# Kernel optimization log

Hardware: AMD Instinct MI355X
Metric: run time of the kernel (lower is better)

## Reference

```python
import jax, jax.numpy as jnp
import numpy as np

B, S, H, SSZ, IN = 1024, 100, 128, 100, 2


def _gru(x, h, Wih, Whh, bih, bhh):
    # PyTorch GRU cell: gates ordered (reset, update, new)
    gx = x @ Wih.T + bih
    gh = h @ Whh.T + bhh
    xr, xz, xn = jnp.split(gx, 3, axis=-1)
    hr, hz, hn = jnp.split(gh, 3, axis=-1)
    r = jax.nn.sigmoid(xr + hr)
    z = jax.nn.sigmoid(xz + hz)
    n = jnp.tanh(xn + r * hn)
    return (1.0 - z) * n + z * h


def _attn(inst_h, rnn_out, W, v):
    # inst_h: [B,S,H], rnn_out: [B,H] -> softmax attention weights [B,S]
    h = jnp.concatenate([inst_h, jnp.broadcast_to(rnn_out[:, None, :], inst_h.shape)], axis=-1)
    s = jax.nn.relu(jnp.einsum('bsk,kh->bsh', h, W)) @ v
    return jax.nn.softmax(s, axis=1)


def setup_inputs() -> dict:
    key = jax.random.key(0)
    k = jax.random.split(key, 32)
    p = lambda i, shape, sc=0.05: sc * jax.random.normal(k[i], shape, jnp.float32)
    instance = jax.random.uniform(k[0], (B, S, IN), jnp.float32)
    # solutions must be per-row permutations of node indices
    solution_1 = jnp.argsort(jax.random.uniform(k[1], (B, S)), axis=1).astype(jnp.int32)
    solution_2 = jnp.argsort(jax.random.uniform(k[2], (B, S)), axis=1).astype(jnp.int32)
    eps = jax.random.normal(k[3], (B, SSZ), jnp.float32)
    return dict(
        instance=instance, solution_1=solution_1, solution_2=solution_2, eps=eps,
        emb_i_W=p(4, (H, IN)), emb_i_b=jnp.zeros(H, jnp.float32),
        emb_r_W=p(5, (H, IN)), emb_r_b=jnp.zeros(H, jnp.float32),
        attn_W=p(6, (2 * H, H)), attn_v=p(7, (H,)),
        gru_Wih=p(8, (3 * H, H)), gru_Whh=p(9, (3 * H, H)),
        gru_bih=jnp.zeros(3 * H, jnp.float32), gru_bhh=jnp.zeros(3 * H, jnp.float32),
        grud_Wih=p(10, (3 * H, 2 * H)), grud_Whh=p(11, (3 * H, H)),
        grud_bih=jnp.zeros(3 * H, jnp.float32), grud_bhh=jnp.zeros(3 * H, jnp.float32),
        enc_fc1_W=p(12, (SSZ, H)), enc_fc1_b=jnp.zeros(SSZ, jnp.float32),
        enc_fc2_W=p(13, (SSZ, H)), enc_fc2_b=jnp.zeros(SSZ, jnp.float32),
        ptr_W=p(14, (2 * H, H)), ptr_v=p(15, (H,)),
        pfc1_W=p(16, (2 * H, 2 * H + SSZ)), pfc1_b=jnp.zeros(2 * H, jnp.float32),
        pfc2_W=p(17, (H, 2 * H)), pfc2_b=jnp.zeros(H, jnp.float32),
    )


def reference(instance, solution_1, solution_2, eps,
              emb_i_W, emb_i_b, emb_r_W, emb_r_b, attn_W, attn_v,
              gru_Wih, gru_Whh, gru_bih, gru_bhh,
              grud_Wih, grud_Whh, grud_bih, grud_bhh,
              enc_fc1_W, enc_fc1_b, enc_fc2_W, enc_fc2_b,
              ptr_W, ptr_v, pfc1_W, pfc1_b, pfc2_W, pfc2_b):
    b_idx = jnp.arange(B)
    inst_h = instance @ emb_i_W.T + emb_i_b  # [B,S,H]
    emb_r = lambda x: x @ emb_r_W.T + emb_r_b
    take = lambda ptr: instance[b_idx, ptr]  # gather node coords [B,IN]

    # ---------------- Encoder ----------------
    def enc_step(carry, ptr):
        h1, h2, ref_h = carry
        h1 = _gru(ref_h, h1, gru_Wih, gru_Whh, gru_bih, gru_bhh)
        a = _attn(inst_h, h1, attn_W, attn_v)
        context = jnp.einsum('bs,bsh->bh', a, inst_h)
        ref_h = emb_r(take(ptr))
        rnn_in = jnp.concatenate([ref_h, context], axis=-1)  # [B,2H]
        h2 = _gru(rnn_in, h2, grud_Wih, grud_Whh, grud_bih, grud_bhh)
        return (h1, h2, ref_h), None

    z0 = jnp.zeros((B, H), instance.dtype)
    ref_h0 = emb_r(take(solution_1[:, 0]))
    (_, h2, _), _ = jax.lax.scan(enc_step, (z0, z0, ref_h0), solution_1[:, 1:].T)
    mu = h2 @ enc_fc1_W.T + enc_fc1_b
    log_var = h2 @ enc_fc2_W.T + enc_fc2_b
    Z = mu + eps * jnp.exp(0.5 * log_var)

    # ---------------- Decoder (teacher forcing) ----------------
    mask0 = jnp.ones((B, S), instance.dtype).at[b_idx, solution_2[:, 0]].set(0.0)

    def dec_step(carry, ptr):
        h1, ref_in, mask = carry
        ref_h = emb_r(ref_in)
        h1 = _gru(ref_h, h1, gru_Wih, gru_Whh, gru_bih, gru_bhh)
        a = _attn(inst_h, h1, attn_W, attn_v)
        context = jnp.einsum('bs,bsh->bh', a, inst_h)
        fc_in = jnp.concatenate([context, Z, ref_h], axis=-1)  # [B, 2H+SSZ]
        fc_out = (fc_in @ pfc1_W.T + pfc1_b) @ pfc2_W.T + pfc2_b  # no activation, as in torch
        hcat = jnp.concatenate([inst_h, jnp.broadcast_to(fc_out[:, None, :], inst_h.shape)], axis=-1)
        logits = jnp.tanh(jnp.einsum('bsk,kh->bsh', hcat, ptr_W)) @ ptr_v  # [B,S]
        probs = jax.nn.softmax(logits + jnp.log(mask), axis=1)
        logp = jnp.log(probs[b_idx, ptr])
        pred = jnp.argmax(probs, axis=1)
        mask = mask.at[b_idx, ptr].set(0.0)  # tsp.update_mask: mark chosen node visited
        return (h1, take(ptr), mask), (pred, logp)

    init = (z0, take(solution_2[:, 0]), mask0)
    _, (preds, logps) = jax.lax.scan(dec_step, init, solution_2[:, 1:].T)
    tour_idx = jnp.concatenate([solution_2[:, :1], preds.T.astype(solution_2.dtype)], axis=1)
    tour_logp = logps.T  # [B, S-1]
    return (mu, log_var, Z, tour_idx, tour_logp)
```

## Files before the change

### kernel.cpp

```cpp
#include <hip/hip_runtime.h>
#include <math.h>

static constexpr int NB  = 1024;
static constexpr int NS  = 100;
static constexpr int NH  = 128;
static constexpr int GPB = 2;
static constexpr int NTHR = 256;
static constexpr int NBLK = NB / GPB;
static constexpr int CH  = 4;

static constexpr int OUT_MU = 0;
static constexpr int OUT_LV = NB * NS;
static constexpr int OUT_Z  = 2 * NB * NS;
static constexpr int OUT_TI = 3 * NB * NS;
static constexpr int OUT_LP = 4 * NB * NS;

#define NEGF (-3.4e38f)

template<int C4>
__device__ __forceinline__ void dot2x3f(const float* __restrict__ wr0,
        const float* __restrict__ wr1, const float* __restrict__ wr2,
        const float* __restrict__ x0, const float* __restrict__ x1,
        float& r00, float& r01, float& r10, float& r11, float& r20, float& r21)
{
    const float4* W0 = reinterpret_cast<const float4*>(wr0);
    const float4* W1 = reinterpret_cast<const float4*>(wr1);
    const float4* W2 = reinterpret_cast<const float4*>(wr2);
    const float4* X0 = reinterpret_cast<const float4*>(x0);
    const float4* X1 = reinterpret_cast<const float4*>(x1);
    float a00 = 0.f, a01 = 0.f, a10 = 0.f, a11 = 0.f, a20 = 0.f, a21 = 0.f;
    #pragma unroll 4
    for (int c = 0; c < C4; ++c) {
        float4 u0 = W0[c], u1 = W1[c], u2 = W2[c];
        float4 v0 = X0[c], v1 = X1[c];
        a00 = fmaf(u0.x, v0.x, a00); a00 = fmaf(u0.y, v0.y, a00); a00 = fmaf(u0.z, v0.z, a00); a00 = fmaf(u0.w, v0.w, a00);
        a01 = fmaf(u0.x, v1.x, a01); a01 = fmaf(u0.y, v1.y, a01); a01 = fmaf(u0.z, v1.z, a01); a01 = fmaf(u0.w, v1.w, a01);
        a10 = fmaf(u1.x, v0.x, a10); a10 = fmaf(u1.y, v0.y, a10); a10 = fmaf(u1.z, v0.z, a10); a10 = fmaf(u1.w, v0.w, a10);
        a11 = fmaf(u1.x, v1.x, a11); a11 = fmaf(u1.y, v1.y, a11); a11 = fmaf(u1.z, v1.z, a11); a11 = fmaf(u1.w, v1.w, a11);
        a20 = fmaf(u2.x, v0.x, a20); a20 = fmaf(u2.y, v0.y, a20); a20 = fmaf(u2.z, v0.z, a20); a20 = fmaf(u2.w, v0.w, a20);
        a21 = fmaf(u2.x, v1.x, a21); a21 = fmaf(u2.y, v1.y, a21); a21 = fmaf(u2.z, v1.z, a21); a21 = fmaf(u2.w, v1.w, a21);
    }
    r00 = a00; r01 = a01; r10 = a10; r11 = a11; r20 = a20; r21 = a21;
}

template<int C4>
__device__ __forceinline__ void dot2f(const float* __restrict__ w,
        const float* __restrict__ x0, const float* __restrict__ x1, float& r0, float& r1)
{
    const float4* W = reinterpret_cast<const float4*>(w);
    const float4* X0 = reinterpret_cast<const float4*>(x0);
    const float4* X1 = reinterpret_cast<const float4*>(x1);
    float a0 = 0.f, a1 = 0.f;
    #pragma unroll 8
    for (int c = 0; c < C4; ++c) {
        float4 u = W[c];
        float4 v0 = X0[c], v1 = X1[c];
        a0 = fmaf(u.x, v0.x, a0); a0 = fmaf(u.y, v0.y, a0); a0 = fmaf(u.z, v0.z, a0); a0 = fmaf(u.w, v0.w, a0);
        a1 = fmaf(u.x, v1.x, a1); a1 = fmaf(u.y, v1.y, a1); a1 = fmaf(u.z, v1.z, a1); a1 = fmaf(u.w, v1.w, a1);
    }
    r0 = a0; r1 = a1;
}

template<int C4>
__device__ __forceinline__ double dotwd(const float* __restrict__ w, const float* __restrict__ x)
{
    const float4* W = reinterpret_cast<const float4*>(w);
    double a = 0.0;
    #pragma unroll 8
    for (int c = 0; c < C4; ++c) {
        float4 u = W[c];
        const float* p = x + 4 * c;
        a = fma((double)u.x, (double)p[0], a);
        a = fma((double)u.y, (double)p[1], a);
        a = fma((double)u.z, (double)p[2], a);
        a = fma((double)u.w, (double)p[3], a);
    }
    return a;
}

__device__ __forceinline__ void gruc(const float* __restrict__ bih, const float* __restrict__ bhh,
        const float* __restrict__ pa, const float* __restrict__ pb, float* __restrict__ h, int j)
{
    double r = 1.0 / (1.0 + exp(-(((double)pa[j]        + (double)bih[j])        + ((double)pb[j]        + (double)bhh[j]))));
    double z = 1.0 / (1.0 + exp(-(((double)pa[NH + j]   + (double)bih[NH + j])   + ((double)pb[NH + j]   + (double)bhh[NH + j]))));
    double n = tanh(((double)pa[2*NH + j] + (double)bih[2*NH + j]) + r * ((double)pb[2*NH + j] + (double)bhh[2*NH + j]));
    h[j] = (float)((1.0 - z) * n + z * (double)h[j]);
}

__device__ __forceinline__ void qhalf(const float* __restrict__ col, int k0,
        const float* __restrict__ hA, const float* __restrict__ hB, double& r0, double& r1)
{
    double a00=0.0,a01=0.0,a02=0.0,a03=0.0;
    double a10=0.0,a11=0.0,a12=0.0,a13=0.0;
    #pragma unroll 8
    for (int k = 0; k < 64; k += 4) {
        float w0 = col[(size_t)(k0+k+0) * NH];
        float w1 = col[(size_t)(k0+k+1) * NH];
        float w2 = col[(size_t)(k0+k+2) * NH];
        float w3 = col[(size_t)(k0+k+3) * NH];
        float4 h0 = *reinterpret_cast<const float4*>(&hA[k0+k]);
        float4 h1v = *reinterpret_cast<const float4*>(&hB[k0+k]);
        a00 = fma((double)w0, (double)h0.x, a00);
        a01 = fma((double)w1, (double)h0.y, a01);
        a02 = fma((double)w2, (double)h0.z, a02);
        a03 = fma((double)w3, (double)h0.w, a03);
        a10 = fma((double)w0, (double)h1v.x, a10);
        a11 = fma((double)w1, (double)h1v.y, a11);
        a12 = fma((double)w2, (double)h1v.z, a12);
        a13 = fma((double)w3, (double)h1v.w, a13);
    }
    r0 = (a00+a01)+(a02+a03); r1 = (a10+a11)+(a12+a13);
}

__device__ __forceinline__ float relu_head(const double* __restrict__ qh,
        const double2* __restrict__ dA, const float* __restrict__ va, float c0v, float c1v)
{
    double c00 = (double)c0v, c10 = (double)c1v;
    double acc0=0.0,acc1=0.0,acc2=0.0,acc3=0.0;
    #pragma unroll 4
    for (int h = 0; h < NH; h += 4) {
        double2 A0=dA[h+0],A1=dA[h+1],A2=dA[h+2],A3=dA[h+3];
        double p0 = fma(c00,A0.x,fma(c10,A0.y,qh[h+0]));
        double p1 = fma(c00,A1.x,fma(c10,A1.y,qh[h+1]));
        double p2 = fma(c00,A2.x,fma(c10,A2.y,qh[h+2]));
        double p3 = fma(c00,A3.x,fma(c10,A3.y,qh[h+3]));
        acc0 = fma(fmax(p0,0.0),(double)va[h+0],acc0);
        acc1 = fma(fmax(p1,0.0),(double)va[h+1],acc1);
        acc2 = fma(fmax(p2,0.0),(double)va[h+2],acc2);
        acc3 = fma(fmax(p3,0.0),(double)va[h+3],acc3);
    }
    return (float)((acc0+acc1)+(acc2+acc3));
}

__device__ __forceinline__ float tanh_head(const double* __restrict__ qh,
        const double2* __restrict__ dA, const float* __restrict__ vp, float c0v, float c1v)
{
    double c00 = (double)c0v, c10 = (double)c1v;
    double acc0=0.0,acc1=0.0,acc2=0.0,acc3=0.0;
    #pragma unroll 4
    for (int h = 0; h < NH; h += 4) {
        double2 A0=dA[h+0],A1=dA[h+1],A2=dA[h+2],A3=dA[h+3];
        double p0 = fma(c00,A0.x,fma(c10,A0.y,qh[h+0]));
        double p1 = fma(c00,A1.x,fma(c10,A1.y,qh[h+1]));
        double p2 = fma(c00,A2.x,fma(c10,A2.y,qh[h+2]));
        double p3 = fma(c00,A3.x,fma(c10,A3.y,qh[h+3]));
        acc0 = fma((double)tanhf((float)p0),(double)vp[h+0],acc0);
        acc1 = fma((double)tanhf((float)p1),(double)vp[h+1],acc1);
        acc2 = fma((double)tanhf((float)p2),(double)vp[h+2],acc2);
        acc3 = fma((double)tanhf((float)p3),(double)vp[h+3],acc3);
    }
    return (float)((acc0+acc1)+(acc2+acc3));
}

__device__ __forceinline__ float ctx_chain(const float* __restrict__ a,
        const float* __restrict__ c0, const float* __restrict__ c1,
        float w0, float w1, float bb)
{
    double a0=0.0,a1=0.0,a2=0.0,a3=0.0;
    #pragma unroll 5
    for (int s = 0; s < NS; s += 4) {
        float ih0 = fmaf(c0[s+0], w0, fmaf(c1[s+0], w1, bb));
        float ih1 = fmaf(c0[s+1], w0, fmaf(c1[s+1], w1, bb));
        float ih2 = fmaf(c0[s+2], w0, fmaf(c1[s+2], w1, bb));
        float ih3 = fmaf(c0[s+3], w0, fmaf(c1[s+3], w1, bb));
        a0 += (double)a[s+0] * (double)ih0;
        a1 += (double)a[s+1] * (double)ih1;
        a2 += (double)a[s+2] * (double)ih2;
        a3 += (double)a[s+3] * (double)ih3;
    }
    return (float)((a0+a1)+(a2+a3));
}

__global__ __launch_bounds__(NTHR) void vae_v21(
    const float* __restrict__ instance, const int* __restrict__ sol1,
    const int* __restrict__ sol2, const float* __restrict__ eps,
    const float* __restrict__ emb_i_W, const float* __restrict__ emb_i_b,
    const float* __restrict__ emb_r_W, const float* __restrict__ emb_r_b,
    const float* __restrict__ attn_W, const float* __restrict__ attn_v,
    const float* __restrict__ gru_Wih, const float* __restrict__ gru_Whh,
    const float* __restrict__ gru_bih, const float* __restrict__ gru_bhh,
    const float* __restrict__ grud_Wih, const float* __restrict__ grud_Whh,
    const float* __restrict__ grud_bih, const float* __restrict__ grud_bhh,
    const float* __restrict__ efc1_W, const float* __restrict__ efc1_b,
    const float* __restrict__ efc2_W, const float* __restrict__ efc2_b,
    const float* __restrict__ ptr_W, const float* __restrict__ ptr_v,
    const float* __restrict__ pfc1_W, const float* __restrict__ pfc1_b,
    const float* __restrict__ pfc2_W, const float* __restrict__ pfc2_b,
    float* __restrict__ out)
{
    __shared__ __align__(16) float  s_x[GPB][360];
    __shared__ __align__(16) float  s_h1[GPB][NH], s_h2[GPB][NH];
    __shared__ float  s_pa[GPB][3 * NH], s_pb[GPB][3 * NH];
    __shared__ double2 dAa[NH], dAp[NH];
    __shared__ double dAba[NH], dAbp[NH];
    __shared__ float  s_c0[GPB][NS], s_c1[GPB][NS];
    __shared__ float  t_wi0[NH], t_wi1[NH], t_bi[NH];
    __shared__ float  t_wr0[NH], t_wr1[NH], t_br[NH];
    __shared__ float  t_va[NH], t_vp[NH];
    __shared__ float  t_gbih[3*NH], t_gbhh[3*NH], t_dbih[3*NH], t_dbhh[3*NH];
    __shared__ float  t_p1b[256], t_p2b[NH];
    __shared__ int    s_sol1[GPB][NS], s_sol2[GPB][NS];
    __shared__ __align__(16) float  s_ref[GPB][NH];
    __shared__ __align__(16) float  h1buf[CH][GPB][NH];
    __shared__ float    rcb0[GPB][CH+1], rcb1[GPB][CH+1];
    __shared__ unsigned maskb[CH][GPB][4], m_run[GPB][4];
    __shared__ __align__(16) double d_qh[CH][GPB][NH];
    __shared__ __align__(16) float  d_pl[2*CH][NS];
    __shared__ __align__(16) float  d_x[2*CH][360];
    __shared__ __align__(16) float  d_fch[2*CH][256];
    __shared__ __align__(16) float  d_fco[CH][GPB][NH];

    const int tid = threadIdx.x;
    const int bbase = blockIdx.x * GPB;
    const int j = tid & (NH - 1);
    const int half = tid >> 7;
    const int g = half;
    const int lane = tid & 63;

    if (tid < NH) {
        t_wi0[tid] = emb_i_W[2*tid]; t_wi1[tid] = emb_i_W[2*tid+1]; t_bi[tid] = emb_i_b[tid];
        t_wr0[tid] = emb_r_W[2*tid]; t_wr1[tid] = emb_r_W[2*tid+1]; t_br[tid] = emb_r_b[tid];
        t_va[tid] = attn_v[tid]; t_vp[tid] = ptr_v[tid];
        t_p2b[tid] = pfc2_b[tid];
    }
    t_p1b[tid] = pfc1_b[tid];
    for (int i = tid; i < 3 * NH; i += NTHR) {
        t_gbih[i] = gru_bih[i]; t_gbhh[i] = gru_bhh[i];
        t_dbih[i] = grud_bih[i]; t_dbhh[i] = grud_bhh[i];
    }
    for (int i = tid; i < GPB * NS; i += NTHR) {
        int gg = i / NS, s = i - gg * NS;
        s_c0[gg][s] = instance[(size_t)((bbase + gg) * NS + s) * 2 + 0];
        s_c1[gg][s] = instance[(size_t)((bbase + gg) * NS + s) * 2 + 1];
        s_sol1[gg][s] = sol1[(bbase + gg) * NS + s];
        s_sol2[gg][s] = sol2[(bbase + gg) * NS + s];
    }
    s_h1[g][j] = 0.f;
    s_h2[g][j] = 0.f;
    __syncthreads();
    {
        const float* Wm = (half == 0) ? attn_W : ptr_W;
        double a0 = 0.0, a1 = 0.0, ab = 0.0;
        for (int k = 0; k < NH; ++k) {
            double wv2 = (double)Wm[(size_t)k * NH + j];
            a0 = fma((double)t_wi0[k], wv2, a0);
            a1 = fma((double)t_wi1[k], wv2, a1);
            ab = fma((double)t_bi[k],  wv2, ab);
        }
        if (half == 0) { dAa[j].x = a0; dAa[j].y = a1; dAba[j] = ab; }
        else           { dAp[j].x = a0; dAp[j].y = a1; dAbp[j] = ab; }
    }
    {
        int sp = s_sol1[g][0];
        s_ref[g][j] = fmaf(s_c0[g][sp], t_wr0[j], fmaf(s_c1[g][sp], t_wr1[j], t_br[j]));
    }
    __syncthreads();

    for (int c = 0; c < (NS - 1 + CH - 1) / CH; ++c) {
        const int t0 = 1 + c * CH;
        const int CHc = (t0 + CH <= NS) ? CH : (NS - t0);
        if (tid < GPB) {
            const int gg = tid;
            for (int qi = 0; qi < CHc; ++qi) {
                int sp = s_sol1[gg][t0 + qi];
                rcb0[gg][qi] = s_c0[gg][sp];
                rcb1[gg][qi] = s_c1[gg][sp];
            }
        }
        __syncthreads();
        for (int q = 0; q < CHc; ++q) {
            if (half == 0) {
                float a00,a01,a10,a11,a20,a21;
                dot2x3f<32>(gru_Wih + (size_t)j * NH, gru_Wih + (size_t)(NH + j) * NH,
                            gru_Wih + (size_t)(2*NH + j) * NH, s_ref[0], s_ref[1],
                            a00,a01,a10,a11,a20,a21);
                s_pa[0][j] = a00;        s_pa[1][j] = a01;
                s_pa[0][NH + j] = a10;   s_pa[1][NH + j] = a11;
                s_pa[0][2*NH + j] = a20; s_pa[1][2*NH + j] = a21;
            } else {
                float a00,a01,a10,a11,a20,a21;
                dot2x3f<32>(gru_Whh + (size_t)j * NH, gru_Whh + (size_t)(NH + j) * NH,
                            gru_Whh + (size_t)(2*NH + j) * NH, s_h1[0], s_h1[1],
                            a00,a01,a10,a11,a20,a21);
                s_pb[0][j] = a00;        s_pb[1][j] = a01;
                s_pb[0][NH + j] = a10;   s_pb[1][NH + j] = a11;
                s_pb[0][2*NH + j] = a20; s_pb[1][2*NH + j] = a21;
            }
            __syncthreads();
            gruc(t_gbih, t_gbhh, s_pa[g], s_pb[g], s_h1[g], j);
            h1buf[q][g][j] = s_h1[g][j];
            s_ref[g][j] = fmaf(rcb0[g][q], t_wr0[j], fmaf(rcb1[g][q], t_wr1[j], t_br[j]));
            __syncthreads();
        }
        {
            const float* col = attn_W + (size_t)NH * NH + j;
            for (int tt = (tid >> 7); tt < CHc; tt += 2) {
                double qA0, qA1, qB0, qB1;
                qhalf(col, 0,  h1buf[tt][0], h1buf[tt][1], qA0, qA1);
                qhalf(col, 64, h1buf[tt][0], h1buf[tt][1], qB0, qB1);
                d_qh[tt][0][j] = dAba[j] + (qA0 + qB0);
                d_qh[tt][1][j] = dAba[j] + (qA1 + qB1);
            }
        }
        __syncthreads();
        for (int idx = tid; idx < 2 * CHc * NS; idx += NTHR) {
            int task = idx / NS, s = idx - task * NS;
            int tt = task >> 1, gg = task & 1;
            d_pl[task][s] = relu_head(d_qh[tt][gg], dAa, t_va, s_c0[gg][s], s_c1[gg][s]);
        }
        __syncthreads();
        {
            int w = tid >> 6;
            for (int task = w; task < 2 * CHc; task += 4) {
                float v1 = d_pl[task][lane];
                bool hasHi = (lane + 64 < NS);
                float v2 = hasHi ? d_pl[task][lane + 64] : NEGF;
                float m = fmaxf(v1, v2);
                m = fmaxf(m, __shfl_xor(m, 32)); m = fmaxf(m, __shfl_xor(m, 16));
                m = fmaxf(m, __shfl_xor(m, 8));  m = fmaxf(m, __shfl_xor(m, 4));
                m = fmaxf(m, __shfl_xor(m, 2));  m = fmaxf(m, __shfl_xor(m, 1));
                float f1 = (float)exp((double)v1 - (double)m);
                float f2 = 0.f;
                if (hasHi) f2 = (float)exp((double)v2 - (double)m);
                double ps = (double)f1 + (double)f2;
                ps += __shfl_xor(ps, 32); ps += __shfl_xor(ps, 16);
                ps += __shfl_xor(ps, 8);  ps += __shfl_xor(ps, 4);
                ps += __shfl_xor(ps, 2);  ps += __shfl_xor(ps, 1);
                d_pl[task][lane] = (float)((double)f1 / ps);
                if (hasHi) d_pl[task][lane + 64] = (float)((double)f2 / ps);
            }
        }
        __syncthreads();
        for (int idx = tid; idx < 2 * CHc * NH; idx += NTHR) {
            int task = idx >> 7, jj = idx & 127;
            int tt = task >> 1, gg = task & 1;
            d_x[task][NH + jj] = ctx_chain(d_pl[task], s_c0[gg], s_c1[gg], t_wi0[jj], t_wi1[jj], t_bi[jj]);
            d_x[task][jj] = fmaf(rcb0[gg][tt], t_wr0[jj], fmaf(rcb1[gg][tt], t_wr1[jj], t_br[jj]));
        }
        __syncthreads();
        for (int q = 0; q < CHc; ++q) {
            if (half == 0) {
                float a00,a01,a10,a11,a20,a21;
                dot2x3f<64>(grud_Wih + (size_t)j * 256, grud_Wih + (size_t)(NH + j) * 256,
                            grud_Wih + (size_t)(2*NH + j) * 256, d_x[2*q], d_x[2*q+1],
                            a00,a01,a10,a11,a20,a21);
                s_pa[0][j] = a00;        s_pa[1][j] = a01;
                s_pa[0][NH + j] = a10;   s_pa[1][NH + j] = a11;
                s_pa[0][2*NH + j] = a20; s_pa[1][2*NH + j] = a21;
            } else {
                float a00,a01,a10,a11,a20,a21;
                dot2x3f<32>(grud_Whh + (size_t)j * NH, grud_Whh + (size_t)(NH + j) * NH,
                            grud_Whh + (size_t)(2*NH + j) * NH, s_h2[0], s_h2[1],
                            a00,a01,a10,a11,a20,a21);
                s_pb[0][j] = a00;        s_pb[1][j] = a01;
                s_pb[0][NH + j] = a10;   s_pb[1][NH + j] = a11;
                s_pb[0][2*NH + j] = a20; s_pb[1][2*NH + j] = a21;
            }
            __syncthreads();
            gruc(t_dbih, t_dbhh, s_pa[g], s_pb[g], s_h2[g], j);
            __syncthreads();
        }
    }

    for (int idx = tid; idx < GPB * NS; idx += NTHR) {
        int gg = idx / NS, s = idx - gg * NS, b = bbase + gg;
        double mu = dotwd<32>(efc1_W + (size_t)s * NH, s_h2[gg]) + (double)efc1_b[s];
        double lv = dotwd<32>(efc2_W + (size_t)s * NH, s_h2[gg]) + (double)efc2_b[s];
        double z  = mu + (double)eps[(size_t)b * NS + s] * exp(0.5 * lv);
        out[OUT_MU + b * NS + s] = (float)mu;
        out[OUT_LV + b * NS + s] = (float)lv;
        out[OUT_Z  + b * NS + s] = (float)z;
        s_x[gg][NH + s] = (float)z;
    }
    s_h1[g][j] = 0.f;
    __syncthreads();
    if (tid < GPB) {
        int b = bbase + tid;
        int s0 = s_sol2[tid][0];
        m_run[tid][0] = 0xFFFFFFFFu; m_run[tid][1] = 0xFFFFFFFFu;
        m_run[tid][2] = 0xFFFFFFFFu; m_run[tid][3] = 0xFu;
        m_run[tid][s0 >> 5] &= ~(1u << (s0 & 31));
        out[OUT_TI + b * NS + 0] = (float)s0;
    }
    __syncthreads();
    {
        int p0 = s_sol2[g][0];
        s_ref[g][j] = fmaf(s_c0[g][p0], t_wr0[j], fmaf(s_c1[g][p0], t_wr1[j], t_br[j]));
    }
    __syncthreads();

    for (int c = 0; c < (NS - 1 + CH - 1) / CH; ++c) {
        const int t0 = 1 + c * CH;
        const int CHc = (t0 + CH <= NS) ? CH : (NS - t0);
        if (tid < GPB) {
            const int gg = tid;
            for (int qi = 0; qi <= CHc; ++qi) {
                int tt = t0 + qi;
                if (qi < CHc) {
                    maskb[qi][gg][0] = m_run[gg][0];
                    maskb[qi][gg][1] = m_run[gg][1];
                    maskb[qi][gg][2] = m_run[gg][2];
                    maskb[qi][gg][3] = m_run[gg][3];
                    int pt = s_sol2[gg][tt];
                    m_run[gg][pt >> 5] &= ~(1u << (pt & 31));
                }
                int sp = s_sol2[gg][tt - 1];
                rcb0[gg][qi] = s_c0[gg][sp];
                rcb1[gg][qi] = s_c1[gg][sp];
            }
        }
        __syncthreads();
        for (int q = 0; q < CHc; ++q) {
            if (half == 0) {
                float a00,a01,a10,a11,a20,a21;
                dot2x3f<32>(gru_Wih + (size_t)j * NH, gru_Wih + (size_t)(NH + j) * NH,
                            gru_Wih + (size_t)(2*NH + j) * NH, s_ref[0], s_ref[1],
                            a00,a01,a10,a11,a20,a21);
                s_pa[0][j] = a00;        s_pa[1][j] = a01;
                s_pa[0][NH + j] = a10;   s_pa[1][NH + j] = a11;
                s_pa[0][2*NH + j] = a20; s_pa[1][2*NH + j] = a21;
            } else {
                float a00,a01,a10,a11,a20,a21;
                dot2x3f<32>(gru_Whh + (size_t)j * NH, gru_Whh + (size_t)(NH + j) * NH,
                            gru_Whh + (size_t)(2*NH + j) * NH, s_h1[0], s_h1[1],
                            a00,a01,a10,a11,a20,a21);
                s_pb[0][j] = a00;        s_pb[1][j] = a01;
                s_pb[0][NH + j] = a10;   s_pb[1][NH + j] = a11;
                s_pb[0][2*NH + j] = a20; s_pb[1][2*NH + j] = a21;
            }
            __syncthreads();
            gruc(t_gbih, t_gbhh, s_pa[g], s_pb[g], s_h1[g], j);
            h1buf[q][g][j] = s_h1[g][j];
            s_ref[g][j] = fmaf(rcb0[g][q+1], t_wr0[j], fmaf(rcb1[g][q+1], t_wr1[j], t_br[j]));
            __syncthreads();
        }
        {
            const float* col = attn_W + (size_t)NH * NH + j;
            for (int tt = (tid >> 7); tt < CHc; tt += 2) {
                double qA0, qA1, qB0, qB1;
                qhalf(col, 0,  h1buf[tt][0], h1buf[tt][1], qA0, qA1);
                qhalf(col, 64, h1buf[tt][0], h1buf[tt][1], qB0, qB1);
                d_qh[tt][0][j] = dAba[j] + (qA0 + qB0);
                d_qh[tt][1][j] = dAba[j] + (qA1 + qB1);
            }
        }
        __syncthreads();
        for (int idx = tid; idx < 2 * CHc * NS; idx += NTHR) {
            int task = idx / NS, s = idx - task * NS;
            int tt = task >> 1, gg = task & 1;
            d_pl[task][s] = relu_head(d_qh[tt][gg], dAa, t_va, s_c0[gg][s], s_c1[gg][s]);
        }
        __syncthreads();
        {
            int w = tid >> 6;
            for (int task = w; task < 2 * CHc; task += 4) {
                float v1 = d_pl[task][lane];
                bool hasHi = (lane + 64 < NS);
                float v2 = hasHi ? d_pl[task][lane + 64] : NEGF;
                float m = fmaxf(v1, v2);
                m = fmaxf(m, __shfl_xor(m, 32)); m = fmaxf(m, __shfl_xor(m, 16));
                m = fmaxf(m, __shfl_xor(m, 8));  m = fmaxf(m, __shfl_xor(m, 4));
                m = fmaxf(m, __shfl_xor(m, 2));  m = fmaxf(m, __shfl_xor(m, 1));
                float f1 = (float)exp((double)v1 - (double)m);
                float f2 = 0.f;
                if (hasHi) f2 = (float)exp((double)v2 - (double)m);
                double ps = (double)f1 + (double)f2;
                ps += __shfl_xor(ps, 32); ps += __shfl_xor(ps, 16);
                ps += __shfl_xor(ps, 8);  ps += __shfl_xor(ps, 4);
                ps += __shfl_xor(ps, 2);  ps += __shfl_xor(ps, 1);
                d_pl[task][lane] = (float)((double)f1 / ps);
                if (hasHi) d_pl[task][lane + 64] = (float)((double)f2 / ps);
            }
        }
        __syncthreads();
        for (int idx = tid; idx < 2 * CHc * NH; idx += NTHR) {
            int task = idx >> 7, jj = idx & 127;
            int tt = task >> 1, gg = task & 1;
            d_x[task][jj] = ctx_chain(d_pl[task], s_c0[gg], s_c1[gg], t_wi0[jj], t_wi1[jj], t_bi[jj]);
            float rc0 = rcb0[gg][tt], rc1 = rcb1[gg][tt];
            d_x[task][228 + jj] = fmaf(rc0, t_wr0[jj], fmaf(rc1, t_wr1[jj], t_br[jj]));
        }
        for (int idx = tid; idx < 2 * CHc * NS; idx += NTHR) {
            int task = idx / NS, s = idx - task * NS;
            int gg = task & 1;
            d_x[task][NH + s] = s_x[gg][NH + s];
        }
        __syncthreads();
        {
            const float* wrow = pfc1_W + (size_t)tid * 356;
            float bb = t_p1b[tid];
            for (int tt = 0; tt < CHc; ++tt) {
                float r0, r1;
                dot2f<89>(wrow, d_x[2*tt], d_x[2*tt+1], r0, r1);
                d_fch[2*tt][tid] = r0 + bb; d_fch[2*tt+1][tid] = r1 + bb;
            }
        }
        __syncthreads();
        {
            const float* wrow = pfc2_W + (size_t)j * 256;
            for (int tt = (tid >> 7); tt < CHc; tt += 2) {
                float r0, r1;
                dot2f<64>(wrow, d_fch[2*tt], d_fch[2*tt+1], r0, r1);
                d_fco[tt][0][j] = r0 + t_p2b[j];
                d_fco[tt][1][j] = r1 + t_p2b[j];
            }
        }
        __syncthreads();
        {
            const float* col = ptr_W + (size_t)NH * NH + j;
            for (int tt = (tid >> 7); tt < CHc; tt += 2) {
                double qA0, qA1, qB0, qB1;
                qhalf(col, 0,  d_fco[tt][0], d_fco[tt][1], qA0, qA1);
                qhalf(col, 64, d_fco[tt][0], d_fco[tt][1], qB0, qB1);
                d_qh[tt][0][j] = dAbp[j] + (qA0 + qB0);
                d_qh[tt][1][j] = dAbp[j] + (qA1 + qB1);
            }
        }
        __syncthreads();
        for (int idx = tid; idx < 2 * CHc * NS; idx += NTHR) {
            int task = idx / NS, s = idx - task * NS;
            int tt = task >> 1, gg = task & 1;
            d_pl[task][s] = tanh_head(d_qh[tt][gg], dAp, t_vp, s_c0[gg][s], s_c1[gg][s]);
        }
        __syncthreads();
        {
            int w = tid >> 6;
            for (int task = w; task < 2 * CHc; task += 4) {
                int tt = task >> 1, gg = task & 1, tstep = t0 + tt;
                const unsigned* mwp = &maskb[tt][gg][0];
                bool u1 = (mwp[lane >> 5] >> (lane & 31)) & 1u;
                float l1 = d_pl[task][lane];
                float c1v = u1 ? l1 : NEGF;
                bool u2 = false; float l2 = 0.f, c2v = NEGF;
                if (lane + 64 < NS) {
                    u2 = (mwp[(lane + 64) >> 5] >> (lane & 31)) & 1u;
                    l2 = d_pl[task][lane + 64];
                    c2v = u2 ? l2 : NEGF;
                }
                float m = fmaxf(c1v, c2v);
                m = fmaxf(m, __shfl_xor(m, 32)); m = fmaxf(m, __shfl_xor(m, 16));
                m = fmaxf(m, __shfl_xor(m, 8));  m = fmaxf(m, __shfl_xor(m, 4));
                m = fmaxf(m, __shfl_xor(m, 2));  m = fmaxf(m, __shfl_xor(m, 1));
                float f1 = u1 ? (float)exp((double)l1 - (double)m) : 0.f;
                float f2 = (lane + 64 < NS && u2) ? (float)exp((double)l2 - (double)m) : 0.f;
                float bv = f1; int bi = lane;
                if (lane + 64 < NS && f2 > bv) { bv = f2; bi = lane + 64; }
                double ps = (double)f1 + (double)f2;
                #pragma unroll
                for (int o = 32; o >= 1; o >>= 1) {
                    float  ov = __shfl_xor(bv, o);
                    int    oi = __shfl_xor(bi, o);
                    double op = __shfl_xor(ps, o);
                    ps += op;
                    if (ov > bv || (ov == bv && oi < bi)) { bv = ov; bi = oi; }
                }
                int pt = s_sol2[gg][tstep];
                float a1s = __shfl(f1, pt & 63);
                float a2s = __shfl(f2, pt & 63);
                float a_pt = (pt < 64) ? a1s : a2s;
                if (lane == 0) {
                    int b2 = bbase + gg;
                    double logp = log((double)a_pt / ps);
                    out[OUT_TI + (size_t)b2 * NS + tstep]             = (float)bi;
                    out[OUT_LP + (size_t)b2 * (NS - 1) + (tstep - 1)] = (float)logp;
                }
            }
        }
        __syncthreads();
    }
}

extern "C" void kernel_launch(void* const* d_in, const int* in_sizes, int n_in,
                              void* d_out, int out_size, void* d_ws, size_t ws_size,
                              hipStream_t stream)
{
    (void)in_sizes; (void)n_in; (void)out_size; (void)d_ws; (void)ws_size;
    vae_v21<<<NBLK, NTHR, 0, stream>>>(
        (const float*)d_in[0], (const int*)d_in[1], (const int*)d_in[2], (const float*)d_in[3],
        (const float*)d_in[4], (const float*)d_in[5], (const float*)d_in[6], (const float*)d_in[7],
        (const float*)d_in[8], (const float*)d_in[9], (const float*)d_in[10], (const float*)d_in[11],
        (const float*)d_in[12], (const float*)d_in[13], (const float*)d_in[14], (const float*)d_in[15],
        (const float*)d_in[16], (const float*)d_in[17], (const float*)d_in[18], (const float*)d_in[19],
        (const float*)d_in[20], (const float*)d_in[21], (const float*)d_in[22], (const float*)d_in[23],
        (const float*)d_in[24], (const float*)d_in[25], (const float*)d_in[26], (const float*)d_in[27],
        (float*)d_out);
}
```

Baseline: 11.58 ms.

## Compute full GRU cell per thread to drop one barrier per step

Each thread now computes all three input-side and hidden-side gate dot products for its own (group, hidden unit) and applies the GRU update in registers. This removes the shared s_pa/s_pb staging and one __syncthreads per recurrent step. Reference embeddings for a whole chunk are precomputed in parallel before the loop, and hidden states are ping-ponged through h1buf. The cost is that each weight row is now read by both groups separately, giving more weight traffic per thread and no reuse of a weight load across the two batch rows.

```diff
diff --git a/kernel.cpp b/kernel.cpp
--- a/kernel.cpp
+++ b/kernel.cpp
@@ -18,29 +18,24 @@
 #define NEGF (-3.4e38f)
 
 template<int C4>
-__device__ __forceinline__ void dot2x3f(const float* __restrict__ wr0,
+__device__ __forceinline__ void dot1x3f(const float* __restrict__ wr0,
         const float* __restrict__ wr1, const float* __restrict__ wr2,
-        const float* __restrict__ x0, const float* __restrict__ x1,
-        float& r00, float& r01, float& r10, float& r11, float& r20, float& r21)
+        const float* __restrict__ x, float& r0, float& r1, float& r2)
 {
     const float4* W0 = reinterpret_cast<const float4*>(wr0);
     const float4* W1 = reinterpret_cast<const float4*>(wr1);
     const float4* W2 = reinterpret_cast<const float4*>(wr2);
-    const float4* X0 = reinterpret_cast<const float4*>(x0);
-    const float4* X1 = reinterpret_cast<const float4*>(x1);
-    float a00 = 0.f, a01 = 0.f, a10 = 0.f, a11 = 0.f, a20 = 0.f, a21 = 0.f;
+    const float4* X  = reinterpret_cast<const float4*>(x);
+    float a0 = 0.f, a1 = 0.f, a2 = 0.f;
     #pragma unroll 4
     for (int c = 0; c < C4; ++c) {
         float4 u0 = W0[c], u1 = W1[c], u2 = W2[c];
-        float4 v0 = X0[c], v1 = X1[c];
-        a00 = fmaf(u0.x, v0.x, a00); a00 = fmaf(u0.y, v0.y, a00); a00 = fmaf(u0.z, v0.z, a00); a00 = fmaf(u0.w, v0.w, a00);
-        a01 = fmaf(u0.x, v1.x, a01); a01 = fmaf(u0.y, v1.y, a01); a01 = fmaf(u0.z, v1.z, a01); a01 = fmaf(u0.w, v1.w, a01);
-        a10 = fmaf(u1.x, v0.x, a10); a10 = fmaf(u1.y, v0.y, a10); a10 = fmaf(u1.z, v0.z, a10); a10 = fmaf(u1.w, v0.w, a10);
-        a11 = fmaf(u1.x, v1.x, a11); a11 = fmaf(u1.y, v1.y, a11); a11 = fmaf(u1.z, v1.z, a11); a11 = fmaf(u1.w, v1.w, a11);
-        a20 = fmaf(u2.x, v0.x, a20); a20 = fmaf(u2.y, v0.y, a20); a20 = fmaf(u2.z, v0.z, a20); a20 = fmaf(u2.w, v0.w, a20);
-        a21 = fmaf(u2.x, v1.x, a21); a21 = fmaf(u2.y, v1.y, a21); a21 = fmaf(u2.z, v1.z, a21); a21 = fmaf(u2.w, v1.w, a21);
-    }
-    r00 = a00; r01 = a01; r10 = a10; r11 = a11; r20 = a20; r21 = a21;
+        float4 v = X[c];
+        a0 = fmaf(u0.x, v.x, a0); a0 = fmaf(u0.y, v.y, a0); a0 = fmaf(u0.z, v.z, a0); a0 = fmaf(u0.w, v.w, a0);
+        a1 = fmaf(u1.x, v.x, a1); a1 = fmaf(u1.y, v.y, a1); a1 = fmaf(u1.z, v.z, a1); a1 = fmaf(u1.w, v.w, a1);
+        a2 = fmaf(u2.x, v.x, a2); a2 = fmaf(u2.y, v.y, a2); a2 = fmaf(u2.z, v.z, a2); a2 = fmaf(u2.w, v.w, a2);
+    }
+    r0 = a0; r1 = a1; r2 = a2;
 }
 
 template<int C4>
@@ -78,13 +73,13 @@
     return a;
 }
 
-__device__ __forceinline__ void gruc(const float* __restrict__ bih, const float* __restrict__ bhh,
-        const float* __restrict__ pa, const float* __restrict__ pb, float* __restrict__ h, int j)
-{
-    double r = 1.0 / (1.0 + exp(-(((double)pa[j]        + (double)bih[j])        + ((double)pb[j]        + (double)bhh[j]))));
-    double z = 1.0 / (1.0 + exp(-(((double)pa[NH + j]   + (double)bih[NH + j])   + ((double)pb[NH + j]   + (double)bhh[NH + j]))));
-    double n = tanh(((double)pa[2*NH + j] + (double)bih[2*NH + j]) + r * ((double)pb[2*NH + j] + (double)bhh[2*NH + j]));
-    h[j] = (float)((1.0 - z) * n + z * (double)h[j]);
+__device__ __forceinline__ float grucr(const float* __restrict__ bih, const float* __restrict__ bhh,
+        float pa0, float pa1, float pa2, float pb0, float pb1, float pb2, float hold, int j)
+{
+    double r = 1.0 / (1.0 + exp(-(((double)pa0 + (double)bih[j])      + ((double)pb0 + (double)bhh[j]))));
+    double z = 1.0 / (1.0 + exp(-(((double)pa1 + (double)bih[NH + j]) + ((double)pb1 + (double)bhh[NH + j]))));
+    double n = tanh(((double)pa2 + (double)bih[2*NH + j]) + r * ((double)pb2 + (double)bhh[2*NH + j]));
+    return (float)((1.0 - z) * n + z * (double)hold);
 }
 
 __device__ __forceinline__ void qhalf(const float* __restrict__ col, int k0,
@@ -171,7 +166,7 @@
     return (float)((a0+a1)+(a2+a3));
 }
 
-__global__ __launch_bounds__(NTHR) void vae_v21(
+__global__ __launch_bounds__(NTHR) void vae_v22(
     const float* __restrict__ instance, const int* __restrict__ sol1,
     const int* __restrict__ sol2, const float* __restrict__ eps,
     const float* __restrict__ emb_i_W, const float* __restrict__ emb_i_b,
@@ -190,7 +185,6 @@
 {
     __shared__ __align__(16) float  s_x[GPB][360];
     __shared__ __align__(16) float  s_h1[GPB][NH], s_h2[GPB][NH];
-    __shared__ float  s_pa[GPB][3 * NH], s_pb[GPB][3 * NH];
     __shared__ double2 dAa[NH], dAp[NH];
     __shared__ double dAba[NH], dAbp[NH];
     __shared__ float  s_c0[GPB][NS], s_c1[GPB][NS];
@@ -200,7 +194,7 @@
     __shared__ float  t_gbih[3*NH], t_gbhh[3*NH], t_dbih[3*NH], t_dbhh[3*NH];
     __shared__ float  t_p1b[256], t_p2b[NH];
     __shared__ int    s_sol1[GPB][NS], s_sol2[GPB][NS];
-    __shared__ __align__(16) float  s_ref[GPB][NH];
+    __shared__ __align__(16) float  refs[CH][GPB][NH];
     __shared__ __align__(16) float  h1buf[CH][GPB][NH];
     __shared__ float    rcb0[GPB][CH+1], rcb1[GPB][CH+1];
     __shared__ unsigned maskb[CH][GPB][4], m_run[GPB][4];
@@ -250,10 +244,6 @@
         if (half == 0) { dAa[j].x = a0; dAa[j].y = a1; dAba[j] = ab; }
         else           { dAp[j].x = a0; dAp[j].y = a1; dAbp[j] = ab; }
     }
-    {
-        int sp = s_sol1[g][0];
-        s_ref[g][j] = fmaf(s_c0[g][sp], t_wr0[j], fmaf(s_c1[g][sp], t_wr1[j], t_br[j]));
-    }
     __syncthreads();
 
     for (int c = 0; c < (NS - 1 + CH - 1) / CH; ++c) {
@@ -267,29 +257,22 @@
                 rcb1[gg][qi] = s_c1[gg][sp];
             }
         }
+        for (int idx = tid; idx < CHc * GPB * NH; idx += NTHR) {
+            int q = idx >> 8, r = idx & 255, gg = r >> 7, jj = r & 127;
+            int sp = s_sol1[gg][t0 + q - 1];
+            refs[q][gg][jj] = fmaf(s_c0[gg][sp], t_wr0[jj], fmaf(s_c1[gg][sp], t_wr1[jj], t_br[jj]));
+        }
         __syncthreads();
         for (int q = 0; q < CHc; ++q) {
-            if (half == 0) {
-                float a00,a01,a10,a11,a20,a21;
-                dot2x3f<32>(gru_Wih + (size_t)j * NH, gru_Wih + (size_t)(NH + j) * NH,
-                            gru_Wih + (size_t)(2*NH + j) * NH, s_ref[0], s_ref[1],
-                            a00,a01,a10,a11,a20,a21);
-                s_pa[0][j] = a00;        s_pa[1][j] = a01;
-                s_pa[0][NH + j] = a10;   s_pa[1][NH + j] = a11;
-                s_pa[0][2*NH + j] = a20; s_pa[1][2*NH + j] = a21;
-            } else {
-                float a00,a01,a10,a11,a20,a21;
-                dot2x3f<32>(gru_Whh + (size_t)j * NH, gru_Whh + (size_t)(NH + j) * NH,
-                            gru_Whh + (size_t)(2*NH + j) * NH, s_h1[0], s_h1[1],
-                            a00,a01,a10,a11,a20,a21);
-                s_pb[0][j] = a00;        s_pb[1][j] = a01;
-                s_pb[0][NH + j] = a10;   s_pb[1][NH + j] = a11;
-                s_pb[0][2*NH + j] = a20; s_pb[1][2*NH + j] = a21;
-            }
-            __syncthreads();
-            gruc(t_gbih, t_gbhh, s_pa[g], s_pb[g], s_h1[g], j);
-            h1buf[q][g][j] = s_h1[g][j];
-            s_ref[g][j] = fmaf(rcb0[g][q], t_wr0[j], fmaf(rcb1[g][q], t_wr1[j], t_br[j]));
+            const float* h1src = (q == 0) ? s_h1[g] : h1buf[q-1][g];
+            float pa0, pa1, pa2, pb0, pb1, pb2;
+            dot1x3f<32>(gru_Wih + (size_t)j * NH, gru_Wih + (size_t)(NH + j) * NH,
+                        gru_Wih + (size_t)(2*NH + j) * NH, refs[q][g], pa0, pa1, pa2);
+            dot1x3f<32>(gru_Whh + (size_t)j * NH, gru_Whh + (size_t)(NH + j) * NH,
+                        gru_Whh + (size_t)(2*NH + j) * NH, h1src, pb0, pb1, pb2);
+            float hn = grucr(t_gbih, t_gbhh, pa0, pa1, pa2, pb0, pb1, pb2, h1src[j], j);
+            h1buf[q][g][j] = hn;
+            if (q == CHc - 1) s_h1[g][j] = hn;
             __syncthreads();
         }
         {
@@ -339,25 +322,14 @@
         }
         __syncthreads();
         for (int q = 0; q < CHc; ++q) {
-            if (half == 0) {
-                float a00,a01,a10,a11,a20,a21;
-                dot2x3f<64>(grud_Wih + (size_t)j * 256, grud_Wih + (size_t)(NH + j) * 256,
-                            grud_Wih + (size_t)(2*NH + j) * 256, d_x[2*q], d_x[2*q+1],
-                            a00,a01,a10,a11,a20,a21);
-                s_pa[0][j] = a00;        s_pa[1][j] = a01;
-                s_pa[0][NH + j] = a10;   s_pa[1][NH + j] = a11;
-                s_pa[0][2*NH + j] = a20; s_pa[1][2*NH + j] = a21;
-            } else {
-                float a00,a01,a10,a11,a20,a21;
-                dot2x3f<32>(grud_Whh + (size_t)j * NH, grud_Whh + (size_t)(NH + j) * NH,
-                            grud_Whh + (size_t)(2*NH + j) * NH, s_h2[0], s_h2[1],
-                            a00,a01,a10,a11,a20,a21);
-                s_pb[0][j] = a00;        s_pb[1][j] = a01;
-                s_pb[0][NH + j] = a10;   s_pb[1][NH + j] = a11;
-                s_pb[0][2*NH + j] = a20; s_pb[1][2*NH + j] = a21;
-            }
-            __syncthreads();
-            gruc(t_dbih, t_dbhh, s_pa[g], s_pb[g], s_h2[g], j);
+            const float* h2src = (q == 0) ? s_h2[g] : h1buf[q-1][g];
+            float pa0, pa1, pa2, pb0, pb1, pb2;
+            dot1x3f<64>(grud_Wih + (size_t)j * 256, grud_Wih + (size_t)(NH + j) * 256,
+                        grud_Wih + (size_t)(2*NH + j) * 256, d_x[2*q + g], pa0, pa1, pa2);
+            dot1x3f<32>(grud_Whh + (size_t)j * NH, grud_Whh + (size_t)(NH + j) * NH,
+                        grud_Whh + (size_t)(2*NH + j) * NH, h2src, pb0, pb1, pb2);
+            float hn = grucr(t_dbih, t_dbhh, pa0, pa1, pa2, pb0, pb1, pb2, h2src[j], j);
+            if (q == CHc - 1) s_h2[g][j] = hn; else h1buf[q][g][j] = hn;
             __syncthreads();
         }
     }
@@ -381,11 +353,6 @@
         m_run[tid][2] = 0xFFFFFFFFu; m_run[tid][3] = 0xFu;
         m_run[tid][s0 >> 5] &= ~(1u << (s0 & 31));
         out[OUT_TI + b * NS + 0] = (float)s0;
-    }
-    __syncthreads();
-    {
-        int p0 = s_sol2[g][0];
-        s_ref[g][j] = fmaf(s_c0[g][p0], t_wr0[j], fmaf(s_c1[g][p0], t_wr1[j], t_br[j]));
     }
     __syncthreads();
 
@@ -409,29 +376,22 @@
                 rcb1[gg][qi] = s_c1[gg][sp];
             }
         }
+        for (int idx = tid; idx < CHc * GPB * NH; idx += NTHR) {
+            int q = idx >> 8, r = idx & 255, gg = r >> 7, jj = r & 127;
+            int sp = s_sol2[gg][t0 + q - 1];
+            refs[q][gg][jj] = fmaf(s_c0[gg][sp], t_wr0[jj], fmaf(s_c1[gg][sp], t_wr1[jj], t_br[jj]));
+        }
         __syncthreads();
         for (int q = 0; q < CHc; ++q) {
-            if (half == 0) {
-                float a00,a01,a10,a11,a20,a21;
-                dot2x3f<32>(gru_Wih + (size_t)j * NH, gru_Wih + (size_t)(NH + j) * NH,
-                            gru_Wih + (size_t)(2*NH + j) * NH, s_ref[0], s_ref[1],
-                            a00,a01,a10,a11,a20,a21);
-                s_pa[0][j] = a00;        s_pa[1][j] = a01;
-                s_pa[0][NH + j] = a10;   s_pa[1][NH + j] = a11;
-                s_pa[0][2*NH + j] = a20; s_pa[1][2*NH + j] = a21;
-            } else {
-                float a00,a01,a10,a11,a20,a21;
-                dot2x3f<32>(gru_Whh + (size_t)j * NH, gru_Whh + (size_t)(NH + j) * NH,
-                            gru_Whh + (size_t)(2*NH + j) * NH, s_h1[0], s_h1[1],
-                            a00,a01,a10,a11,a20,a21);
-                s_pb[0][j] = a00;        s_pb[1][j] = a01;
-                s_pb[0][NH + j] = a10;   s_pb[1][NH + j] = a11;
-                s_pb[0][2*NH + j] = a20; s_pb[1][2*NH + j] = a21;
-            }
-            __syncthreads();
-            gruc(t_gbih, t_gbhh, s_pa[g], s_pb[g], s_h1[g], j);
-            h1buf[q][g][j] = s_h1[g][j];
-            s_ref[g][j] = fmaf(rcb0[g][q+1], t_wr0[j], fmaf(rcb1[g][q+1], t_wr1[j], t_br[j]));
+            const float* h1src = (q == 0) ? s_h1[g] : h1buf[q-1][g];
+            float pa0, pa1, pa2, pb0, pb1, pb2;
+            dot1x3f<32>(gru_Wih + (size_t)j * NH, gru_Wih + (size_t)(NH + j) * NH,
+                        gru_Wih + (size_t)(2*NH + j) * NH, refs[q][g], pa0, pa1, pa2);
+            dot1x3f<32>(gru_Whh + (size_t)j * NH, gru_Whh + (size_t)(NH + j) * NH,
+                        gru_Whh + (size_t)(2*NH + j) * NH, h1src, pb0, pb1, pb2);
+            float hn = grucr(t_gbih, t_gbhh, pa0, pa1, pa2, pb0, pb1, pb2, h1src[j], j);
+            h1buf[q][g][j] = hn;
+            if (q == CHc - 1) s_h1[g][j] = hn;
             __syncthreads();
         }
         {
@@ -575,7 +535,7 @@
                               hipStream_t stream)
 {
     (void)in_sizes; (void)n_in; (void)out_size; (void)d_ws; (void)ws_size;
-    vae_v21<<<NBLK, NTHR, 0, stream>>>(
+    vae_v22<<<NBLK, NTHR, 0, stream>>>(
         (const float*)d_in[0], (const int*)d_in[1], (const int*)d_in[2], (const float*)d_in[3],
         (const float*)d_in[4], (const float*)d_in[5], (const float*)d_in[6], (const float*)d_in[7],
         (const float*)d_in[8], (const float*)d_in[9], (const float*)d_in[10], (const float*)d_in[11],
```

After: 18.52 ms. 59.8% more time.
